# Performance work log

Hardware: AMD Instinct MI355X
Metric: run time of the kernel (lower is better)

The kernel has to match this reference:

```python
import jax, jax.numpy as jnp
import numpy as np

N, D, S, C, H = 65536, 512, 32, 64, 64  # batch, input_size, n_subnets, cols/subnet, hidden
GROUP = 32  # columns per predictor group


def _build_col_ids():
    # 16 groups of 32 cols; interactions = (i,i+1) and (i,i+2) mod 16
    pairs = [(i, (i + 1) % 16) for i in range(16)] + [(i, (i + 2) % 16) for i in range(16)]
    ids = np.array([np.concatenate([np.arange(a * GROUP, (a + 1) * GROUP),
                                    np.arange(b * GROUP, (b + 1) * GROUP)])
                    for a, b in pairs], dtype=np.int32)  # [S, C]
    return jnp.asarray(ids)


def setup_inputs() -> dict:
    key = jax.random.key(0)
    ks = jax.random.split(key, 7)
    scale = 0.05  # keep log_rate inside clamp range most of the time
    return {
        "x": jax.random.normal(ks[0], (N, D), jnp.float32),
        "skip_w": jax.random.normal(ks[1], (D,), jnp.float32) * scale,
        "skip_b": jax.random.normal(ks[2], (1,), jnp.float32) * scale,
        "W1": jax.random.normal(ks[3], (S, C, H), jnp.float32) * scale,
        "b1": jax.random.normal(ks[4], (S, H), jnp.float32) * scale,
        "W2": jax.random.normal(ks[5], (S, H), jnp.float32) * scale,
        "b2": jax.random.normal(ks[6], (S,), jnp.float32) * scale,
        "col_ids": _build_col_ids(),
    }


def reference(x, skip_w, skip_b, W1, b1, W2, b2, col_ids):
    # skip: Linear(D,1) then squeeze -> [N]
    log_rate = x @ skip_w + skip_b[0]
    # fused gather + batched tiny MLP over all S subnets
    xg = x[:, col_ids]                                  # [N, S, C]
    h = jax.nn.relu(jnp.einsum('nsc,sch->nsh', xg, W1) + b1)  # [N, S, H]
    out = jnp.einsum('nsh,sh->ns', h, W2) + b2          # [N, S]
    log_rate = log_rate + out.sum(axis=-1)
    return jnp.clip(log_rate, -20.0, 20.0)
```

## Files before the change

### kernel.cpp

```cpp
#include <hip/hip_runtime.h>

#define NROWS 65536
#define DCOLS 512

typedef float  f32x4  __attribute__((ext_vector_type(4)));
typedef __bf16 bf16x8 __attribute__((ext_vector_type(8)));

__device__ __forceinline__ unsigned short f2bf(float f) {
    unsigned int u = __builtin_bit_cast(unsigned int, f);
    u += 0x7fffu + ((u >> 16) & 1u);
    return (unsigned short)(u >> 16);
}

__global__ void pack_kernel(const float* __restrict__ W1,
                            const float* __restrict__ b1,
                            const float* __restrict__ W2,
                            unsigned short* __restrict__ w1p,
                            float2* __restrict__ pk) {
    int idx  = blockIdx.x * 256 + threadIdx.x;
    int j    = idx & 7;
    int lane = (idx >> 3) & 63;
    int f    = (idx >> 9) & 7;
    int s    = idx >> 12;
    int kt = f >> 2, nt = f & 3;
    int c = kt * 32 + (lane >> 4) * 8 + j;
    int h = nt * 16 + (lane & 15);
    w1p[idx] = f2bf(W1[(s * 64 + c) * 64 + h]);
    if (idx < 2048) pk[idx] = make_float2(b1[idx], W2[idx]);
}

__launch_bounds__(256, 2)
__global__ void fused_kernel(const float* __restrict__ x,
                             const float* __restrict__ skip_w,
                             const float* __restrict__ skip_b,
                             const float* __restrict__ b2,
                             const unsigned short* __restrict__ w1p,
                             const float2* __restrict__ pk,
                             float* __restrict__ out) {
    __shared__ uint4 w1buf[2][512];

    const int tid  = threadIdx.x;
    const int wave = tid >> 6;
    const int lane = tid & 63;
    const int m    = lane & 15;
    const int q    = lane >> 4;
    const int row0 = blockIdx.x * 128 + wave * 32;

    uint4 afr[2][16];
    float sp[2] = {0.f, 0.f};
#pragma unroll
    for (int g = 0; g < 16; ++g) {
        const float4 sw0 = *(const float4*)(skip_w + g * 32 + q * 8);
        const float4 sw1 = *(const float4*)(skip_w + g * 32 + q * 8 + 4);
#pragma unroll
        for (int mt = 0; mt < 2; ++mt) {
            const float* xp = x + (long)(row0 + mt * 16 + m) * DCOLS + g * 32 + q * 8;
            const float4 a0 = *(const float4*)(xp);
            const float4 a1 = *(const float4*)(xp + 4);
            float s0 = fmaf(a0.x, sw0.x, fmaf(a0.y, sw0.y, fmaf(a0.z, sw0.z, a0.w * sw0.w)));
            float s1 = fmaf(a1.x, sw1.x, fmaf(a1.y, sw1.y, fmaf(a1.z, sw1.z, a1.w * sw1.w)));
            sp[mt] += s0 + s1;
            unsigned int u01 = (unsigned int)f2bf(a0.x) | ((unsigned int)f2bf(a0.y) << 16);
            unsigned int u23 = (unsigned int)f2bf(a0.z) | ((unsigned int)f2bf(a0.w) << 16);
            unsigned int u45 = (unsigned int)f2bf(a1.x) | ((unsigned int)f2bf(a1.y) << 16);
            unsigned int u67 = (unsigned int)f2bf(a1.z) | ((unsigned int)f2bf(a1.w) << 16);
            afr[mt][g] = make_uint4(u01, u23, u45, u67);
        }
    }
    float sf[2];
#pragma unroll
    for (int mt = 0; mt < 2; ++mt) {
        float v = sp[mt];
        v += __shfl_xor(v, 16);
        v += __shfl_xor(v, 32);
        sf[mt] = v;
    }

    float b2s = 0.f;
#pragma unroll
    for (int i = 0; i < 32; ++i) b2s += b2[i];
    const float sb0 = skip_b[0];

    const uint4* wp = (const uint4*)w1p;
    float part[2][4] = {{0.f,0.f,0.f,0.f},{0.f,0.f,0.f,0.f}};

    w1buf[0][tid]       = wp[tid];
    w1buf[0][tid + 256] = wp[tid + 256];
    __syncthreads();

#pragma unroll
    for (int s = 0; s < 32; ++s) {
        const int cb = s & 1, nb = cb ^ 1;
        if (s + 1 < 32) {
            w1buf[nb][tid]       = wp[(s + 1) * 512 + tid];
            w1buf[nb][tid + 256] = wp[(s + 1) * 512 + tid + 256];
        }
        const int ga = s & 15;
        const int gb = ((s & 15) + 1 + (s >> 4)) & 15;

        bf16x8 bfr[2][4];
#pragma unroll
        for (int kt = 0; kt < 2; ++kt)
#pragma unroll
            for (int nt = 0; nt < 4; ++nt)
                bfr[kt][nt] = __builtin_bit_cast(bf16x8, w1buf[cb][(kt * 4 + nt) * 64 + lane]);

        f32x4 acc[2][4];
#pragma unroll
        for (int mt = 0; mt < 2; ++mt) {
            const bf16x8 a0 = __builtin_bit_cast(bf16x8, afr[mt][ga]);
            const bf16x8 a1 = __builtin_bit_cast(bf16x8, afr[mt][gb]);
#pragma unroll
            for (int nt = 0; nt < 4; ++nt) {
                f32x4 z = {0.f, 0.f, 0.f, 0.f};
                acc[mt][nt] = __builtin_amdgcn_mfma_f32_16x16x32_bf16(a0, bfr[0][nt], z, 0, 0, 0);
                acc[mt][nt] = __builtin_amdgcn_mfma_f32_16x16x32_bf16(a1, bfr[1][nt], acc[mt][nt], 0, 0, 0);
            }
        }

#pragma unroll
        for (int nt = 0; nt < 4; ++nt) {
            const float2 bw = pk[s * 64 + nt * 16 + m];
#pragma unroll
            for (int mt = 0; mt < 2; ++mt)
#pragma unroll
                for (int r = 0; r < 4; ++r) {
                    float h = acc[mt][nt][r] + bw.x;
                    h = fmaxf(h, 0.f);
                    part[mt][r] = fmaf(h, bw.y, part[mt][r]);
                }
        }
        __syncthreads();
    }

#pragma unroll
    for (int mt = 0; mt < 2; ++mt)
#pragma unroll
        for (int r = 0; r < 4; ++r) {
            float v = part[mt][r];
            v += __shfl_xor(v, 1);
            v += __shfl_xor(v, 2);
            v += __shfl_xor(v, 4);
            v += __shfl_xor(v, 8);
            const float skipv = __shfl(sf[mt], q * 4 + r);
            float val = v + b2s + sb0 + skipv;
            val = fminf(fmaxf(val, -20.f), 20.f);
            if (m == 0) out[row0 + mt * 16 + q * 4 + r] = val;
        }
}

extern "C" void kernel_launch(void* const* d_in, const int* in_sizes, int n_in,
                              void* d_out, int out_size, void* d_ws, size_t ws_size,
                              hipStream_t stream) {
    const float* x      = (const float*)d_in[0];
    const float* skip_w = (const float*)d_in[1];
    const float* skip_b = (const float*)d_in[2];
    const float* W1     = (const float*)d_in[3];
    const float* b1     = (const float*)d_in[4];
    const float* W2     = (const float*)d_in[5];
    const float* b2     = (const float*)d_in[6];

    unsigned short* w1p = (unsigned short*)d_ws;
    float2* pk = (float2*)((char*)d_ws + 262144);

    pack_kernel<<<512, 256, 0, stream>>>(W1, b1, W2, w1p, pk);
    fused_kernel<<<NROWS / 128, 256, 0, stream>>>(x, skip_w, skip_b, b2, w1p, pk,
                                                  (float*)d_out);
}
```

Measured before the change: 225.4 us.

## Stage x rows through LDS with async global_load_lds and swizzled layout

Replaces the direct strided global loads of x (each lane reading 32B pieces across rows) with asynchronous global_load_lds transfers into a per-wave double-buffered, XOR-swizzled LDS region, then reads fragments from LDS. W1 tiles are also streamed straight into LDS with global_load_lds, and the pack kernel is rewritten to read W1 coalesced and scatter writes. The aim is better coalescing and more overlap of x loading with conversion work. In exchange LDS use grows to about 66KB per block, which may limit occupancy to fewer blocks per CU, and the wait counts are hand-tuned.

```diff
diff --git a/kernel.cpp b/kernel.cpp
--- a/kernel.cpp
+++ b/kernel.cpp
@@ -11,21 +11,26 @@
     u += 0x7fffu + ((u >> 16) & 1u);
     return (unsigned short)(u >> 16);
 }
+
+#define GLOAD_LDS16(gp, lp)                                                   \
+    __builtin_amdgcn_global_load_lds(                                         \
+        (__attribute__((address_space(1))) void*)(gp),                        \
+        (__attribute__((address_space(3))) void*)(lp), 16, 0, 0)
 
 __global__ void pack_kernel(const float* __restrict__ W1,
                             const float* __restrict__ b1,
                             const float* __restrict__ W2,
                             unsigned short* __restrict__ w1p,
                             float2* __restrict__ pk) {
-    int idx  = blockIdx.x * 256 + threadIdx.x;
-    int j    = idx & 7;
-    int lane = (idx >> 3) & 63;
-    int f    = (idx >> 9) & 7;
-    int s    = idx >> 12;
-    int kt = f >> 2, nt = f & 3;
-    int c = kt * 32 + (lane >> 4) * 8 + j;
-    int h = nt * 16 + (lane & 15);
-    w1p[idx] = f2bf(W1[(s * 64 + c) * 64 + h]);
+    int idx = blockIdx.x * 256 + threadIdx.x;
+    int s = idx >> 12;
+    int c = (idx >> 6) & 63;
+    int h = idx & 63;
+    int kt = c >> 5, nt = h >> 4;
+    int lane = (((c & 31) >> 3) << 4) | (h & 15);
+    int j = c & 7;
+    int dst = (s << 12) | (((kt << 2) | nt) << 9) | (lane << 3) | j;
+    w1p[dst] = f2bf(W1[idx]);
     if (idx < 2048) pk[idx] = make_float2(b1[idx], W2[idx]);
 }
 
@@ -37,7 +42,7 @@
                              const unsigned short* __restrict__ w1p,
                              const float2* __restrict__ pk,
                              float* __restrict__ out) {
-    __shared__ uint4 w1buf[2][512];
+    __shared__ char smem[67584] __attribute__((aligned(128)));
 
     const int tid  = threadIdx.x;
     const int wave = tid >> 6;
@@ -46,25 +51,56 @@
     const int q    = lane >> 4;
     const int row0 = blockIdx.x * 128 + wave * 32;
 
+    char*  xw  = smem + wave * 16384;
+    float* swl = (float*)(smem + 65536);
+    uint4* w1b = (uint4*)smem;
+
+    auto issue_chunk = [&](int k, int b) {
+#pragma unroll
+        for (int i = 0; i < 8; ++i) {
+            const int r   = i * 4 + (lane >> 4);
+            const int col = k * 64 + 4 * ((lane & 15) ^ (r & 7));
+            const float* src = x + (long)(row0 + r) * DCOLS + col;
+            GLOAD_LDS16(src, xw + b * 8192 + i * 1024);
+        }
+    };
+
+    issue_chunk(0, 0);
+    issue_chunk(1, 1);
+    swl[tid]       = skip_w[tid];
+    swl[tid + 256] = skip_w[tid + 256];
+    __syncthreads();
+
     uint4 afr[2][16];
     float sp[2] = {0.f, 0.f};
-#pragma unroll
-    for (int g = 0; g < 16; ++g) {
-        const float4 sw0 = *(const float4*)(skip_w + g * 32 + q * 8);
-        const float4 sw1 = *(const float4*)(skip_w + g * 32 + q * 8 + 4);
+    const int sz = (m & 7) << 4;
+#pragma unroll
+    for (int k = 0; k < 8; ++k) {
+        if (k >= 2) asm volatile("s_waitcnt vmcnt(8)" ::: "memory");
+        const char* cbuf = xw + (k & 1) * 8192;
 #pragma unroll
         for (int mt = 0; mt < 2; ++mt) {
-            const float* xp = x + (long)(row0 + mt * 16 + m) * DCOLS + g * 32 + q * 8;
-            const float4 a0 = *(const float4*)(xp);
-            const float4 a1 = *(const float4*)(xp + 4);
-            float s0 = fmaf(a0.x, sw0.x, fmaf(a0.y, sw0.y, fmaf(a0.z, sw0.z, a0.w * sw0.w)));
-            float s1 = fmaf(a1.x, sw1.x, fmaf(a1.y, sw1.y, fmaf(a1.z, sw1.z, a1.w * sw1.w)));
-            sp[mt] += s0 + s1;
-            unsigned int u01 = (unsigned int)f2bf(a0.x) | ((unsigned int)f2bf(a0.y) << 16);
-            unsigned int u23 = (unsigned int)f2bf(a0.z) | ((unsigned int)f2bf(a0.w) << 16);
-            unsigned int u45 = (unsigned int)f2bf(a1.x) | ((unsigned int)f2bf(a1.y) << 16);
-            unsigned int u67 = (unsigned int)f2bf(a1.z) | ((unsigned int)f2bf(a1.w) << 16);
-            afr[mt][g] = make_uint4(u01, u23, u45, u67);
+            const char* rb = cbuf + (mt * 16 + m) * 256;
+#pragma unroll
+            for (int gh = 0; gh < 2; ++gh) {
+                const int o = gh * 128 + q * 32;
+                const float4 va = *(const float4*)(rb + (o ^ sz));
+                const float4 vb = *(const float4*)(rb + ((o + 16) ^ sz));
+                const float4 s0 = *(const float4*)(swl + k * 64 + gh * 32 + q * 8);
+                const float4 s1 = *(const float4*)(swl + k * 64 + gh * 32 + q * 8 + 4);
+                float d = fmaf(va.x, s0.x, fmaf(va.y, s0.y, fmaf(va.z, s0.z, va.w * s0.w)));
+                d = fmaf(vb.x, s1.x, fmaf(vb.y, s1.y, fmaf(vb.z, s1.z, fmaf(vb.w, s1.w, d))));
+                sp[mt] += d;
+                unsigned int u01 = (unsigned int)f2bf(va.x) | ((unsigned int)f2bf(va.y) << 16);
+                unsigned int u23 = (unsigned int)f2bf(va.z) | ((unsigned int)f2bf(va.w) << 16);
+                unsigned int u45 = (unsigned int)f2bf(vb.x) | ((unsigned int)f2bf(vb.y) << 16);
+                unsigned int u67 = (unsigned int)f2bf(vb.z) | ((unsigned int)f2bf(vb.w) << 16);
+                afr[mt][2 * k + gh] = make_uint4(u01, u23, u45, u67);
+            }
+        }
+        if (k + 2 < 8) {
+            asm volatile("s_waitcnt lgkmcnt(0)" ::: "memory");
+            issue_chunk(k + 2, k & 1);
         }
     }
     float sf[2];
@@ -81,29 +117,30 @@
     for (int i = 0; i < 32; ++i) b2s += b2[i];
     const float sb0 = skip_b[0];
 
+    __syncthreads();
     const uint4* wp = (const uint4*)w1p;
+    GLOAD_LDS16(wp + tid,       w1b + wave * 64);
+    GLOAD_LDS16(wp + 256 + tid, w1b + 256 + wave * 64);
+    __syncthreads();
+
     float part[2][4] = {{0.f,0.f,0.f,0.f},{0.f,0.f,0.f,0.f}};
 
-    w1buf[0][tid]       = wp[tid];
-    w1buf[0][tid + 256] = wp[tid + 256];
-    __syncthreads();
-
 #pragma unroll
     for (int s = 0; s < 32; ++s) {
-        const int cb = s & 1, nb = cb ^ 1;
+        const int cbf = (s & 1) * 512, nbf = cbf ^ 512;
         if (s + 1 < 32) {
-            w1buf[nb][tid]       = wp[(s + 1) * 512 + tid];
-            w1buf[nb][tid + 256] = wp[(s + 1) * 512 + tid + 256];
+            GLOAD_LDS16(wp + (s + 1) * 512 + tid,       w1b + nbf + wave * 64);
+            GLOAD_LDS16(wp + (s + 1) * 512 + 256 + tid, w1b + nbf + 256 + wave * 64);
         }
         const int ga = s & 15;
-        const int gb = ((s & 15) + 1 + (s >> 4)) & 15;
+        const int gb = (ga + 1 + (s >> 4)) & 15;
 
         bf16x8 bfr[2][4];
 #pragma unroll
         for (int kt = 0; kt < 2; ++kt)
 #pragma unroll
             for (int nt = 0; nt < 4; ++nt)
-                bfr[kt][nt] = __builtin_bit_cast(bf16x8, w1buf[cb][(kt * 4 + nt) * 64 + lane]);
+                bfr[kt][nt] = __builtin_bit_cast(bf16x8, w1b[cbf + (kt * 4 + nt) * 64 + lane]);
 
         f32x4 acc[2][4];
 #pragma unroll
```

New measurement: 228.2 us. About the same (+1.3%).

## Stream W1 into LDS via direct global-to-LDS loads in 4-subnet chunks

Applied to the files above, without the earlier changes.

Replaces register-staged W1 copies into shared memory with global_load_lds direct transfers, and groups four subnets per double-buffered stage, cutting barriers from 32 to 8. The first stage's load is issued before the x loading so it overlaps with that work. The pack kernel is also rewritten to read W1 coalesced and scatter the writes. LDS use grows to 64 KB per block, which may limit occupancy under the 2-block launch bound, and correctness relies on how the async load places data per wave.

```diff
diff --git a/kernel.cpp b/kernel.cpp
--- a/kernel.cpp
+++ b/kernel.cpp
@@ -12,20 +12,25 @@
     return (unsigned short)(u >> 16);
 }
 
+#define GLOAD_LDS16(gp, lp)                                                   \
+    __builtin_amdgcn_global_load_lds(                                         \
+        (__attribute__((address_space(1))) void*)(gp),                        \
+        (__attribute__((address_space(3))) void*)(lp), 16, 0, 0)
+
 __global__ void pack_kernel(const float* __restrict__ W1,
                             const float* __restrict__ b1,
                             const float* __restrict__ W2,
                             unsigned short* __restrict__ w1p,
                             float2* __restrict__ pk) {
-    int idx  = blockIdx.x * 256 + threadIdx.x;
-    int j    = idx & 7;
-    int lane = (idx >> 3) & 63;
-    int f    = (idx >> 9) & 7;
-    int s    = idx >> 12;
-    int kt = f >> 2, nt = f & 3;
-    int c = kt * 32 + (lane >> 4) * 8 + j;
-    int h = nt * 16 + (lane & 15);
-    w1p[idx] = f2bf(W1[(s * 64 + c) * 64 + h]);
+    int idx = blockIdx.x * 256 + threadIdx.x;
+    int s = idx >> 12;
+    int c = (idx >> 6) & 63;
+    int h = idx & 63;
+    int kt = c >> 5, nt = h >> 4;
+    int lane = (((c & 31) >> 3) << 4) | (h & 15);
+    int j = c & 7;
+    int dst = (s << 12) | (((kt << 2) | nt) << 9) | (lane << 3) | j;
+    w1p[dst] = f2bf(W1[idx]);
     if (idx < 2048) pk[idx] = make_float2(b1[idx], W2[idx]);
 }
 
@@ -37,7 +42,7 @@
                              const unsigned short* __restrict__ w1p,
                              const float2* __restrict__ pk,
                              float* __restrict__ out) {
-    __shared__ uint4 w1buf[2][512];
+    __shared__ uint4 w1buf[2][2048];
 
     const int tid  = threadIdx.x;
     const int wave = tid >> 6;
@@ -45,6 +50,12 @@
     const int m    = lane & 15;
     const int q    = lane >> 4;
     const int row0 = blockIdx.x * 128 + wave * 32;
+
+    const uint4* wp = (const uint4*)w1p;
+
+#pragma unroll
+    for (int i = 0; i < 8; ++i)
+        GLOAD_LDS16(wp + i * 256 + tid, &w1buf[0][i * 256 + wave * 64]);
 
     uint4 afr[2][16];
     float sp[2] = {0.f, 0.f};
@@ -81,54 +92,58 @@
     for (int i = 0; i < 32; ++i) b2s += b2[i];
     const float sb0 = skip_b[0];
 
-    const uint4* wp = (const uint4*)w1p;
     float part[2][4] = {{0.f,0.f,0.f,0.f},{0.f,0.f,0.f,0.f}};
 
-    w1buf[0][tid]       = wp[tid];
-    w1buf[0][tid + 256] = wp[tid + 256];
     __syncthreads();
 
 #pragma unroll
-    for (int s = 0; s < 32; ++s) {
-        const int cb = s & 1, nb = cb ^ 1;
-        if (s + 1 < 32) {
-            w1buf[nb][tid]       = wp[(s + 1) * 512 + tid];
-            w1buf[nb][tid + 256] = wp[(s + 1) * 512 + tid + 256];
+    for (int g = 0; g < 8; ++g) {
+        const int cb = g & 1, nb = cb ^ 1;
+        if (g + 1 < 8) {
+#pragma unroll
+            for (int i = 0; i < 8; ++i)
+                GLOAD_LDS16(wp + (g + 1) * 2048 + i * 256 + tid,
+                            &w1buf[nb][i * 256 + wave * 64]);
         }
-        const int ga = s & 15;
-        const int gb = ((s & 15) + 1 + (s >> 4)) & 15;
+#pragma unroll
+        for (int ss = 0; ss < 4; ++ss) {
+            const int s  = g * 4 + ss;
+            const int ga = s & 15;
+            const int gb = (ga + 1 + (s >> 4)) & 15;
+            const uint4* wb = &w1buf[cb][ss * 512];
 
-        bf16x8 bfr[2][4];
+            bf16x8 bfr[2][4];
 #pragma unroll
-        for (int kt = 0; kt < 2; ++kt)
+            for (int kt = 0; kt < 2; ++kt)
 #pragma unroll
-            for (int nt = 0; nt < 4; ++nt)
-                bfr[kt][nt] = __builtin_bit_cast(bf16x8, w1buf[cb][(kt * 4 + nt) * 64 + lane]);
+                for (int nt = 0; nt < 4; ++nt)
+                    bfr[kt][nt] = __builtin_bit_cast(bf16x8, wb[(kt * 4 + nt) * 64 + lane]);
 
-        f32x4 acc[2][4];
+            f32x4 acc[2][4];
 #pragma unroll
-        for (int mt = 0; mt < 2; ++mt) {
-            const bf16x8 a0 = __builtin_bit_cast(bf16x8, afr[mt][ga]);
-            const bf16x8 a1 = __builtin_bit_cast(bf16x8, afr[mt][gb]);
+            for (int mt = 0; mt < 2; ++mt) {
+                const bf16x8 a0 = __builtin_bit_cast(bf16x8, afr[mt][ga]);
+                const bf16x8 a1 = __builtin_bit_cast(bf16x8, afr[mt][gb]);
+#pragma unroll
+                for (int nt = 0; nt < 4; ++nt) {
+                    f32x4 z = {0.f, 0.f, 0.f, 0.f};
+                    acc[mt][nt] = __builtin_amdgcn_mfma_f32_16x16x32_bf16(a0, bfr[0][nt], z, 0, 0, 0);
+                    acc[mt][nt] = __builtin_amdgcn_mfma_f32_16x16x32_bf16(a1, bfr[1][nt], acc[mt][nt], 0, 0, 0);
+                }
+            }
+
 #pragma unroll
             for (int nt = 0; nt < 4; ++nt) {
-                f32x4 z = {0.f, 0.f, 0.f, 0.f};
-                acc[mt][nt] = __builtin_amdgcn_mfma_f32_16x16x32_bf16(a0, bfr[0][nt], z, 0, 0, 0);
-                acc[mt][nt] = __builtin_amdgcn_mfma_f32_16x16x32_bf16(a1, bfr[1][nt], acc[mt][nt], 0, 0, 0);
+                const float2 bw = pk[s * 64 + nt * 16 + m];
+#pragma unroll
+                for (int mt = 0; mt < 2; ++mt)
+#pragma unroll
+                    for (int r = 0; r < 4; ++r) {
+                        float h = acc[mt][nt][r] + bw.x;
+                        h = fmaxf(h, 0.f);
+                        part[mt][r] = fmaf(h, bw.y, part[mt][r]);
+                    }
             }
-        }
-
-#pragma unroll
-        for (int nt = 0; nt < 4; ++nt) {
-            const float2 bw = pk[s * 64 + nt * 16 + m];
-#pragma unroll
-            for (int mt = 0; mt < 2; ++mt)
-#pragma unroll
-                for (int r = 0; r < 4; ++r) {
-                    float h = acc[mt][nt][r] + bw.x;
-                    h = fmaxf(h, 0.f);
-                    part[mt][r] = fmaf(h, bw.y, part[mt][r]);
-                }
         }
         __syncthreads();
     }
```

After: 227.2 us. No clear change (+0.8%).
